# Kernel optimization log

Measured on AMD Instinct MI355X. Metric: run time of the kernel, lower is better.

The kernel has to match this reference:

```python
import jax, jax.numpy as jnp
import numpy as np


def setup_inputs() -> dict:
    key = jax.random.key(0)
    k1, k2 = jax.random.split(key)
    B, S_ENC, S_DEC, D = 8, 2048, 2048, 1024
    enc_outputs = jax.random.normal(k1, (B, S_ENC, D), dtype=jnp.float32)
    dec_outputs = jax.random.normal(k2, (B, S_DEC, D), dtype=jnp.float32)
    return {"enc_outputs": enc_outputs, "dec_outputs": dec_outputs}


def reference(enc_outputs, dec_outputs):
    # scores: [B, S_enc, S_dec] = enc @ dec^T (unscaled)
    a_t = jnp.einsum('bed,btd->bet', enc_outputs, dec_outputs)
    a_t = jax.nn.softmax(a_t, axis=-1)
    # context: [B, S_dec, D] = a_t^T @ enc
    c_t = jnp.einsum('bet,bed->btd', a_t, enc_outputs)
    return c_t
```

## Files before the change

### kernel.cpp

```cpp
#include <hip/hip_runtime.h>


typedef _Float16 half8 __attribute__((ext_vector_type(8)));
typedef _Float16 half4v __attribute__((ext_vector_type(4)));
typedef float floatx4 __attribute__((ext_vector_type(4)));

#define BM 128
#define BN 128
#define BK 32

__device__ __forceinline__ void async_load16(const _Float16* g, void* l) {
  __builtin_amdgcn_global_load_lds(
      (const __attribute__((address_space(1))) void*)g,
      (__attribute__((address_space(3))) void*)l, 16, 0, 0);
}

template <typename OutT>
__global__ __launch_bounds__(256, 2) void gemm_bt(
    const _Float16* __restrict__ A, const _Float16* __restrict__ Bt,
    OutT* __restrict__ C, int K, long strideA, long strideB, long strideC,
    int ldA, int ldB, int ldC) {
  __shared__ _Float16 lds_a[BM * BK];
  __shared__ _Float16 lds_b[BN * BK];

  const int b = blockIdx.z;
  A += (long)b * strideA;
  Bt += (long)b * strideB;
  C += (long)b * strideC;
  const int m0 = blockIdx.y * BM;
  const int n0 = blockIdx.x * BN;
  const int tid = threadIdx.x;
  const int lane = tid & 63;
  const int wave = tid >> 6;
  const int quad = lane >> 4;
  const int l16 = lane & 15;
  const int wm = (wave >> 1) * 64;
  const int wn = (wave & 1) * 64;

  floatx4 acc[4][4] = {};

  for (int k0 = 0; k0 < K; k0 += BK) {
#pragma unroll
    for (int c = 0; c < 2; ++c) {
      const int off = c * 4096 + wave * 1024 + lane * 16;
      const int row = off >> 6;
      const int ke = (off & 63) >> 1;
      async_load16(A + (long)(m0 + row) * ldA + k0 + ke, (char*)lds_a + off);
      async_load16(Bt + (long)(n0 + row) * ldB + k0 + ke, (char*)lds_b + off);
    }
    __syncthreads();

    half8 af[4], bf[4];
#pragma unroll
    for (int i = 0; i < 4; ++i) {
      af[i] = *(const half8*)&lds_a[(wm + i * 16 + l16) * BK + quad * 8];
      bf[i] = *(const half8*)&lds_b[(wn + i * 16 + l16) * BK + quad * 8];
    }
#pragma unroll
    for (int i = 0; i < 4; ++i)
#pragma unroll
      for (int j = 0; j < 4; ++j)
        acc[i][j] = __builtin_amdgcn_mfma_f32_16x16x32_f16(af[i], bf[j],
                                                           acc[i][j], 0, 0, 0);
    __syncthreads();
  }

#pragma unroll
  for (int i = 0; i < 4; ++i) {
    const int r0 = m0 + wm + i * 16 + quad * 4;
#pragma unroll
    for (int j = 0; j < 4; ++j) {
      const int col = n0 + wn + j * 16 + l16;
#pragma unroll
      for (int r = 0; r < 4; ++r)
        C[(long)(r0 + r) * ldC + col] = (OutT)acc[i][j][r];
    }
  }
}

__global__ __launch_bounds__(256) void conv_enc(const float* __restrict__ E,
                                                _Float16* __restrict__ Eh,
                                                _Float16* __restrict__ EhT,
                                                int Se, int D) {
  __shared__ _Float16 tile[64][72];
  const int b = blockIdx.z;
  const int d0 = blockIdx.x * 64;
  const int e0 = blockIdx.y * 64;
  const float* Eb = E + (size_t)b * Se * D;
  _Float16* Ehb = Eh + (size_t)b * Se * D;
  _Float16* EhTb = EhT + (size_t)b * D * Se;
  const int tid = threadIdx.x;
  const int lr = tid >> 4;
  const int lc = (tid & 15) * 4;
#pragma unroll
  for (int r = 0; r < 4; ++r) {
    const int e = e0 + lr + r * 16;
    float4 v = *(const float4*)(Eb + (size_t)e * D + d0 + lc);
    half4v h;
    h[0] = (_Float16)v.x; h[1] = (_Float16)v.y;
    h[2] = (_Float16)v.z; h[3] = (_Float16)v.w;
    *(half4v*)(Ehb + (size_t)e * D + d0 + lc) = h;
#pragma unroll
    for (int j = 0; j < 4; ++j) tile[lc + j][lr + r * 16] = h[j];
  }
  __syncthreads();
#pragma unroll
  for (int r = 0; r < 4; ++r) {
    const int d = lr + r * 16;
    half4v w;
#pragma unroll
    for (int j = 0; j < 4; ++j) w[j] = tile[d][lc + j];
    *(half4v*)(EhTb + (size_t)(d0 + d) * Se + e0 + lc) = w;
  }
}

__global__ __launch_bounds__(256) void conv_dec(const float* __restrict__ X,
                                                _Float16* __restrict__ Y) {
  const size_t i = ((size_t)blockIdx.x * 256 + threadIdx.x) * 4;
  float4 v = *(const float4*)(X + i);
  half4v h;
  h[0] = (_Float16)v.x; h[1] = (_Float16)v.y;
  h[2] = (_Float16)v.z; h[3] = (_Float16)v.w;
  *(half4v*)(Y + i) = h;
}

__global__ __launch_bounds__(256) void row_stats(const _Float16* __restrict__ S,
                                                 float2* __restrict__ stats) {
  __shared__ float red[8];
  const long row = blockIdx.x;
  const _Float16* p = S + row * 2048;
  const int tid = threadIdx.x;
  const int wave = tid >> 6, lane = tid & 63;

  half8 v = *(const half8*)(p + tid * 8);
  float f[8];
#pragma unroll
  for (int j = 0; j < 8; ++j) f[j] = (float)v[j];

  float mx = f[0];
#pragma unroll
  for (int j = 1; j < 8; ++j) mx = fmaxf(mx, f[j]);
  for (int o = 32; o; o >>= 1) mx = fmaxf(mx, __shfl_xor(mx, o, 64));
  if (lane == 0) red[wave] = mx;
  __syncthreads();
  if (tid == 0)
    red[4] = fmaxf(fmaxf(red[0], red[1]), fmaxf(red[2], red[3]));
  __syncthreads();
  mx = red[4];

  float s = 0.f;
#pragma unroll
  for (int j = 0; j < 8; ++j) s += __expf(f[j] - mx);
  for (int o = 32; o; o >>= 1) s += __shfl_xor(s, o, 64);
  if (lane == 0) red[wave] = s;
  __syncthreads();
  if (tid == 0) {
    const float tot = red[0] + red[1] + red[2] + red[3];
    stats[row] = make_float2(mx, 1.0f / tot);
  }
}

__global__ __launch_bounds__(256) void norm_transpose(
    const _Float16* __restrict__ S, const float2* __restrict__ stats,
    _Float16* __restrict__ PT, int Se, int St) {
  __shared__ _Float16 tile[64][72];
  const int b = blockIdx.z;
  const int t0 = blockIdx.x * 64;
  const int e0 = blockIdx.y * 64;
  const _Float16* Sb = S + (size_t)b * Se * St;
  _Float16* Pb = PT + (size_t)b * St * Se;
  const float2* stb = stats + (size_t)b * Se;
  const int tid = threadIdx.x;
  const int lr = tid >> 4;
  const int lc = (tid & 15) * 4;
#pragma unroll
  for (int r = 0; r < 4; ++r) {
    const int e = lr + r * 16;
    const float2 st = stb[e0 + e];
    half4v v = *(const half4v*)(Sb + (size_t)(e0 + e) * St + t0 + lc);
#pragma unroll
    for (int j = 0; j < 4; ++j) {
      const float pv = __expf((float)v[j] - st.x) * st.y;
      tile[lc + j][e] = (_Float16)pv;
    }
  }
  __syncthreads();
#pragma unroll
  for (int r = 0; r < 4; ++r) {
    const int t = lr + r * 16;
    half4v w;
#pragma unroll
    for (int j = 0; j < 4; ++j) w[j] = tile[t][lc + j];
    *(half4v*)(Pb + (size_t)(t0 + t) * Se + e0 + lc) = w;
  }
}

extern "C" void kernel_launch(void* const* d_in, const int* in_sizes, int n_in,
                              void* d_out, int out_size, void* d_ws,
                              size_t ws_size, hipStream_t stream) {
  const float* enc = (const float*)d_in[0];
  const float* dec = (const float*)d_in[1];
  float* out = (float*)d_out;

  const int B = 8, SE = 2048, SD = 2048, D = 1024;
  char* ws = (char*)d_ws;
  _Float16* enc_h = (_Float16*)ws;
  _Float16* dec_h = (_Float16*)(ws + 33554432);
  _Float16* PT = (_Float16*)ws;
  _Float16* enc_hT = (_Float16*)(ws + 67108864);
  _Float16* S_h = (_Float16*)(ws + 100663296);
  float2* stats = (float2*)(ws + 167772160);

  conv_enc<<<dim3(D / 64, SE / 64, B), 256, 0, stream>>>(enc, enc_h, enc_hT,
                                                         SE, D);
  conv_dec<<<dim3((size_t)B * SD * D / 1024), 256, 0, stream>>>(dec, dec_h);
  gemm_bt<_Float16><<<dim3(SD / BN, SE / BM, B), 256, 0, stream>>>(
      enc_h, dec_h, S_h, D, (long)SE * D, (long)SD * D, (long)SE * SD, D, D,
      SD);
  row_stats<<<dim3(B * SE), 256, 0, stream>>>(S_h, stats);
  norm_transpose<<<dim3(SD / 64, SE / 64, B), 256, 0, stream>>>(S_h, stats, PT,
                                                                SE, SD);
  gemm_bt<float><<<dim3(D / BN, SD / BM, B), 256, 0, stream>>>(
      PT, enc_hT, out, SE, (long)SD * SE, (long)D * SE, (long)SD * D, SE, SE,
      D);
}
```

Before: 395.8 us.

## Switch GEMM to 32x32 MFMA with swizzled LDS, XCD-aware tile mapping, and vectorized helpers

The GEMM now uses 32x32x16 MFMA instructions and stores its LDS tiles with an XOR swizzle so that fragment reads avoid bank conflicts. Blocks are remapped so that each XCD works on a contiguous group of output tiles, which should improve L2 reuse. The transpose kernels now build 4x4 register transposes and write wider 16-byte stores, conv_dec handles 8 elements per thread, and row_stats assigns one wave per row with no block-level barriers. The block remap assumes particular grid shapes (16x16 and 8x16 tiles per batch), so it is tied to these problem sizes.

```diff
diff --git a/kernel.cpp b/kernel.cpp
--- a/kernel.cpp
+++ b/kernel.cpp
@@ -3,7 +3,7 @@
 
 typedef _Float16 half8 __attribute__((ext_vector_type(8)));
 typedef _Float16 half4v __attribute__((ext_vector_type(4)));
-typedef float floatx4 __attribute__((ext_vector_type(4)));
+typedef float floatx16 __attribute__((ext_vector_type(16)));
 
 #define BM 128
 #define BN 128
@@ -15,7 +15,7 @@
       (__attribute__((address_space(3))) void*)l, 16, 0, 0);
 }
 
-template <typename OutT>
+template <typename OutT, int RN>
 __global__ __launch_bounds__(256, 2) void gemm_bt(
     const _Float16* __restrict__ A, const _Float16* __restrict__ Bt,
     OutT* __restrict__ C, int K, long strideA, long strideB, long strideC,
@@ -27,53 +27,73 @@
   A += (long)b * strideA;
   Bt += (long)b * strideB;
   C += (long)b * strideC;
-  const int m0 = blockIdx.y * BM;
-  const int n0 = blockIdx.x * BN;
+
+  const int id = blockIdx.y * gridDim.x + blockIdx.x;
+  const int xcd = id & 7;
+  const int l = id >> 3;
+  const int by = (xcd & 3) * 4 + l / RN;
+  const int bx = (xcd >> 2) * RN + l % RN;
+  const int m0 = by * BM;
+  const int n0 = bx * BN;
+
   const int tid = threadIdx.x;
   const int lane = tid & 63;
   const int wave = tid >> 6;
-  const int quad = lane >> 4;
-  const int l16 = lane & 15;
+  const int l31 = lane & 31;
+  const int kh = lane >> 5;
   const int wm = (wave >> 1) * 64;
   const int wn = (wave & 1) * 64;
 
-  floatx4 acc[4][4] = {};
+  floatx16 acc[2][2] = {};
 
   for (int k0 = 0; k0 < K; k0 += BK) {
 #pragma unroll
     for (int c = 0; c < 2; ++c) {
       const int off = c * 4096 + wave * 1024 + lane * 16;
       const int row = off >> 6;
-      const int ke = (off & 63) >> 1;
+      const int ke = (((off >> 4) & 3) ^ (row & 3)) * 8;
       async_load16(A + (long)(m0 + row) * ldA + k0 + ke, (char*)lds_a + off);
       async_load16(Bt + (long)(n0 + row) * ldB + k0 + ke, (char*)lds_b + off);
     }
     __syncthreads();
 
-    half8 af[4], bf[4];
-#pragma unroll
-    for (int i = 0; i < 4; ++i) {
-      af[i] = *(const half8*)&lds_a[(wm + i * 16 + l16) * BK + quad * 8];
-      bf[i] = *(const half8*)&lds_b[(wn + i * 16 + l16) * BK + quad * 8];
+    half8 af[2][2], bf[2][2];
+#pragma unroll
+    for (int i = 0; i < 2; ++i) {
+      const int ra = wm + i * 32 + l31;
+      const int rb = wn + i * 32 + l31;
+#pragma unroll
+      for (int s = 0; s < 2; ++s) {
+        const int ck = s * 2 + kh;
+        af[i][s] = *(const half8*)((const char*)lds_a + ra * 64 +
+                                   ((ck ^ (ra & 3)) << 4));
+        bf[i][s] = *(const half8*)((const char*)lds_b + rb * 64 +
+                                   ((ck ^ (rb & 3)) << 4));
+      }
     }
 #pragma unroll
-    for (int i = 0; i < 4; ++i)
-#pragma unroll
-      for (int j = 0; j < 4; ++j)
-        acc[i][j] = __builtin_amdgcn_mfma_f32_16x16x32_f16(af[i], bf[j],
-                                                           acc[i][j], 0, 0, 0);
+    for (int s = 0; s < 2; ++s)
+#pragma unroll
+      for (int i = 0; i < 2; ++i)
+#pragma unroll
+        for (int j = 0; j < 2; ++j)
+          acc[i][j] = __builtin_amdgcn_mfma_f32_32x32x16_f16(
+              af[i][s], bf[j][s], acc[i][j], 0, 0, 0);
     __syncthreads();
   }
 
 #pragma unroll
-  for (int i = 0; i < 4; ++i) {
-    const int r0 = m0 + wm + i * 16 + quad * 4;
-#pragma unroll
-    for (int j = 0; j < 4; ++j) {
-      const int col = n0 + wn + j * 16 + l16;
-#pragma unroll
-      for (int r = 0; r < 4; ++r)
-        C[(long)(r0 + r) * ldC + col] = (OutT)acc[i][j][r];
+  for (int i = 0; i < 2; ++i) {
+    const int r_base = m0 + wm + i * 32 + 4 * kh;
+#pragma unroll
+    for (int j = 0; j < 2; ++j) {
+      const int col = n0 + wn + j * 32 + l31;
+#pragma unroll
+      for (int g = 0; g < 4; ++g)
+#pragma unroll
+        for (int rr = 0; rr < 4; ++rr)
+          C[(long)(r_base + g * 8 + rr) * ldC + col] =
+              (OutT)acc[i][j][g * 4 + rr];
     }
   }
 }
@@ -82,7 +102,7 @@
                                                 _Float16* __restrict__ Eh,
                                                 _Float16* __restrict__ EhT,
                                                 int Se, int D) {
-  __shared__ _Float16 tile[64][72];
+  __shared__ _Float16 T[64][72];
   const int b = blockIdx.z;
   const int d0 = blockIdx.x * 64;
   const int e0 = blockIdx.y * 64;
@@ -90,80 +110,77 @@
   _Float16* Ehb = Eh + (size_t)b * Se * D;
   _Float16* EhTb = EhT + (size_t)b * D * Se;
   const int tid = threadIdx.x;
-  const int lr = tid >> 4;
-  const int lc = (tid & 15) * 4;
+  const int tx = tid & 15;
+  const int ty = tid >> 4;
+
+  half4v h[4];
 #pragma unroll
   for (int r = 0; r < 4; ++r) {
-    const int e = e0 + lr + r * 16;
-    float4 v = *(const float4*)(Eb + (size_t)e * D + d0 + lc);
-    half4v h;
-    h[0] = (_Float16)v.x; h[1] = (_Float16)v.y;
-    h[2] = (_Float16)v.z; h[3] = (_Float16)v.w;
-    *(half4v*)(Ehb + (size_t)e * D + d0 + lc) = h;
-#pragma unroll
-    for (int j = 0; j < 4; ++j) tile[lc + j][lr + r * 16] = h[j];
+    const int e = e0 + ty * 4 + r;
+    float4 v = *(const float4*)(Eb + (size_t)e * D + d0 + tx * 4);
+    h[r][0] = (_Float16)v.x; h[r][1] = (_Float16)v.y;
+    h[r][2] = (_Float16)v.z; h[r][3] = (_Float16)v.w;
+    *(half4v*)(Ehb + (size_t)e * D + d0 + tx * 4) = h[r];
+  }
+#pragma unroll
+  for (int c = 0; c < 4; ++c) {
+    half4v w;
+#pragma unroll
+    for (int r = 0; r < 4; ++r) w[r] = h[r][c];
+    *(half4v*)&T[tx * 4 + c][ty * 4] = w;
   }
   __syncthreads();
 #pragma unroll
-  for (int r = 0; r < 4; ++r) {
-    const int d = lr + r * 16;
-    half4v w;
-#pragma unroll
-    for (int j = 0; j < 4; ++j) w[j] = tile[d][lc + j];
-    *(half4v*)(EhTb + (size_t)(d0 + d) * Se + e0 + lc) = w;
+  for (int p = 0; p < 2; ++p) {
+    const int idx = tid + p * 256;
+    const int row = idx >> 3;
+    const int ck = idx & 7;
+    *(half8*)(EhTb + (size_t)(d0 + row) * Se + e0 + ck * 8) =
+        *(const half8*)&T[row][ck * 8];
   }
 }
 
 __global__ __launch_bounds__(256) void conv_dec(const float* __restrict__ X,
                                                 _Float16* __restrict__ Y) {
-  const size_t i = ((size_t)blockIdx.x * 256 + threadIdx.x) * 4;
-  float4 v = *(const float4*)(X + i);
-  half4v h;
-  h[0] = (_Float16)v.x; h[1] = (_Float16)v.y;
-  h[2] = (_Float16)v.z; h[3] = (_Float16)v.w;
-  *(half4v*)(Y + i) = h;
+  const size_t i = ((size_t)blockIdx.x * 256 + threadIdx.x) * 8;
+  float4 a = *(const float4*)(X + i);
+  float4 b = *(const float4*)(X + i + 4);
+  half8 h;
+  h[0] = (_Float16)a.x; h[1] = (_Float16)a.y;
+  h[2] = (_Float16)a.z; h[3] = (_Float16)a.w;
+  h[4] = (_Float16)b.x; h[5] = (_Float16)b.y;
+  h[6] = (_Float16)b.z; h[7] = (_Float16)b.w;
+  *(half8*)(Y + i) = h;
 }
 
 __global__ __launch_bounds__(256) void row_stats(const _Float16* __restrict__ S,
                                                  float2* __restrict__ stats) {
-  __shared__ float red[8];
-  const long row = blockIdx.x;
+  const int lane = threadIdx.x & 63;
+  const long row = (long)blockIdx.x * 4 + (threadIdx.x >> 6);
   const _Float16* p = S + row * 2048;
-  const int tid = threadIdx.x;
-  const int wave = tid >> 6, lane = tid & 63;
-
-  half8 v = *(const half8*)(p + tid * 8);
-  float f[8];
-#pragma unroll
-  for (int j = 0; j < 8; ++j) f[j] = (float)v[j];
-
+
+  float f[32];
+#pragma unroll
+  for (int q = 0; q < 4; ++q) {
+    half8 v = *(const half8*)(p + q * 512 + lane * 8);
+#pragma unroll
+    for (int j = 0; j < 8; ++j) f[q * 8 + j] = (float)v[j];
+  }
   float mx = f[0];
 #pragma unroll
-  for (int j = 1; j < 8; ++j) mx = fmaxf(mx, f[j]);
+  for (int j = 1; j < 32; ++j) mx = fmaxf(mx, f[j]);
   for (int o = 32; o; o >>= 1) mx = fmaxf(mx, __shfl_xor(mx, o, 64));
-  if (lane == 0) red[wave] = mx;
-  __syncthreads();
-  if (tid == 0)
-    red[4] = fmaxf(fmaxf(red[0], red[1]), fmaxf(red[2], red[3]));
-  __syncthreads();
-  mx = red[4];
-
   float s = 0.f;
 #pragma unroll
-  for (int j = 0; j < 8; ++j) s += __expf(f[j] - mx);
+  for (int j = 0; j < 32; ++j) s += __expf(f[j] - mx);
   for (int o = 32; o; o >>= 1) s += __shfl_xor(s, o, 64);
-  if (lane == 0) red[wave] = s;
-  __syncthreads();
-  if (tid == 0) {
-    const float tot = red[0] + red[1] + red[2] + red[3];
-    stats[row] = make_float2(mx, 1.0f / tot);
-  }
+  if (lane == 0) stats[row] = make_float2(mx, 1.0f / s);
 }
 
 __global__ __launch_bounds__(256) void norm_transpose(
     const _Float16* __restrict__ S, const float2* __restrict__ stats,
     _Float16* __restrict__ PT, int Se, int St) {
-  __shared__ _Float16 tile[64][72];
+  __shared__ _Float16 T[64][72];
   const int b = blockIdx.z;
   const int t0 = blockIdx.x * 64;
   const int e0 = blockIdx.y * 64;
@@ -171,27 +188,34 @@
   _Float16* Pb = PT + (size_t)b * St * Se;
   const float2* stb = stats + (size_t)b * Se;
   const int tid = threadIdx.x;
-  const int lr = tid >> 4;
-  const int lc = (tid & 15) * 4;
+  const int tx = tid & 15;
+  const int ty = tid >> 4;
+
+  half4v pr[4];
 #pragma unroll
   for (int r = 0; r < 4; ++r) {
-    const int e = lr + r * 16;
-    const float2 st = stb[e0 + e];
-    half4v v = *(const half4v*)(Sb + (size_t)(e0 + e) * St + t0 + lc);
-#pragma unroll
-    for (int j = 0; j < 4; ++j) {
-      const float pv = __expf((float)v[j] - st.x) * st.y;
-      tile[lc + j][e] = (_Float16)pv;
-    }
+    const int e = e0 + ty * 4 + r;
+    const float2 st = stb[e];
+    half4v v = *(const half4v*)(Sb + (size_t)e * St + t0 + tx * 4);
+#pragma unroll
+    for (int c = 0; c < 4; ++c)
+      pr[r][c] = (_Float16)(__expf((float)v[c] - st.x) * st.y);
+  }
+#pragma unroll
+  for (int c = 0; c < 4; ++c) {
+    half4v w;
+#pragma unroll
+    for (int r = 0; r < 4; ++r) w[r] = pr[r][c];
+    *(half4v*)&T[tx * 4 + c][ty * 4] = w;
   }
   __syncthreads();
 #pragma unroll
-  for (int r = 0; r < 4; ++r) {
-    const int t = lr + r * 16;
-    half4v w;
-#pragma unroll
-    for (int j = 0; j < 4; ++j) w[j] = tile[t][lc + j];
-    *(half4v*)(Pb + (size_t)(t0 + t) * Se + e0 + lc) = w;
+  for (int p = 0; p < 2; ++p) {
+    const int idx = tid + p * 256;
+    const int row = idx >> 3;
+    const int ck = idx & 7;
+    *(half8*)(Pb + (size_t)(t0 + row) * Se + e0 + ck * 8) =
+        *(const half8*)&T[row][ck * 8];
   }
 }
 
@@ -213,14 +237,14 @@
 
   conv_enc<<<dim3(D / 64, SE / 64, B), 256, 0, stream>>>(enc, enc_h, enc_hT,
                                                          SE, D);
-  conv_dec<<<dim3((size_t)B * SD * D / 1024), 256, 0, stream>>>(dec, dec_h);
-  gemm_bt<_Float16><<<dim3(SD / BN, SE / BM, B), 256, 0, stream>>>(
+  conv_dec<<<dim3((size_t)B * SD * D / 2048), 256, 0, stream>>>(dec, dec_h);
+  gemm_bt<_Float16, 8><<<dim3(SD / BN, SE / BM, B), 256, 0, stream>>>(
       enc_h, dec_h, S_h, D, (long)SE * D, (long)SD * D, (long)SE * SD, D, D,
       SD);
-  row_stats<<<dim3(B * SE), 256, 0, stream>>>(S_h, stats);
+  row_stats<<<dim3(B * SE / 4), 256, 0, stream>>>(S_h, stats);
   norm_transpose<<<dim3(SD / 64, SE / 64, B), 256, 0, stream>>>(S_h, stats, PT,
                                                                 SE, SD);
-  gemm_bt<float><<<dim3(D / BN, SD / BM, B), 256, 0, stream>>>(
+  gemm_bt<float, 4><<<dim3(D / BN, SD / BM, B), 256, 0, stream>>>(
       PT, enc_hT, out, SE, (long)SD * SE, (long)D * SE, (long)SD * D, SE, SE,
       D);
 }
```

After: 376.2 us. 1.05x faster.
